# Optimization experiments

Hardware: AMD Instinct MI355X
Metric: run time of the kernel (lower is better)

The kernel has to match this reference:

```python
import jax, jax.numpy as jnp
import numpy as np

N = 25000; E = 100000; H = 64; NODE_IN = 32; EDGE_IN = 16; L = 3


def _lin(key, fan_in, fan_out):
    kw, kb = jax.random.split(key)
    s = 1.0 / np.sqrt(fan_in)
    W = jax.random.uniform(kw, (fan_out, fan_in), minval=-s, maxval=s, dtype=jnp.float32)
    b = jax.random.uniform(kb, (fan_out,), minval=-s, maxval=s, dtype=jnp.float32)
    return W, b


def setup_inputs() -> dict:
    key = jax.random.key(0)
    ks = jax.random.split(key, 16)
    x = jax.random.normal(ks[0], (N, NODE_IN), dtype=jnp.float32)
    edge_attr = jax.random.normal(ks[1], (E, EDGE_IN), dtype=jnp.float32)
    edge_index = jax.random.randint(ks[2], (2, E), 0, N, dtype=jnp.int32)
    Wn1, bn1 = _lin(ks[3], NODE_IN, H)
    Wn2, bn2 = _lin(ks[4], H, H)
    Wn3, bn3 = _lin(ks[5], H, H)
    We1, be1 = _lin(ks[6], EDGE_IN, H)
    We2, be2 = _lin(ks[7], H, H)
    We3, be3 = _lin(ks[8], H, H * H)
    roots = jax.random.normal(ks[9], (L, H, H), dtype=jnp.float32) / np.sqrt(H)
    conv_bias = jnp.zeros((L, H), dtype=jnp.float32)
    s = 1.0 / np.sqrt(H)
    gru_Wih = jax.random.uniform(ks[10], (3 * H, H), minval=-s, maxval=s, dtype=jnp.float32)
    gru_Whh = jax.random.uniform(ks[11], (3 * H, H), minval=-s, maxval=s, dtype=jnp.float32)
    gru_bih = jax.random.uniform(ks[12], (3 * H,), minval=-s, maxval=s, dtype=jnp.float32)
    gru_bhh = jax.random.uniform(ks[13], (3 * H,), minval=-s, maxval=s, dtype=jnp.float32)
    return dict(x=x, edge_attr=edge_attr,
                Wn1=Wn1, bn1=bn1, Wn2=Wn2, bn2=bn2, Wn3=Wn3, bn3=bn3,
                We1=We1, be1=be1, We2=We2, be2=be2, We3=We3, be3=be3,
                roots=roots, conv_bias=conv_bias,
                gru_Wih=gru_Wih, gru_Whh=gru_Whh, gru_bih=gru_bih, gru_bhh=gru_bhh,
                edge_index=edge_index)


def _mpnn_forward(x, edge_attr, Wn1, bn1, Wn2, bn2, Wn3, bn3,
                  We1, be1, We2, be2, We3, be3,
                  roots, conv_bias, gru_Wih, gru_Whh, gru_bih, gru_bhh, edge_index):
    src, dst = edge_index[0], edge_index[1]
    # mlp_in: Linear-ReLU-Linear-ReLU-Linear
    h = jax.nn.relu(x @ Wn1.T + bn1)
    h = jax.nn.relu(h @ Wn2.T + bn2)
    h = h @ Wn3.T + bn3  # [N, H]
    # edge MLP is shared across all NNConv layers and edge_attr is constant -> compute once
    ew = jax.nn.relu(edge_attr @ We1.T + be1)
    ew = jax.nn.relu(ew @ We2.T + be2)
    ew = (ew @ We3.T + be3).reshape(E, H, H)  # per-edge weight [E, in, out]
    hidden = jnp.zeros((x.shape[0], H), dtype=h.dtype)  # GRU hidden (1 layer)
    for l in range(L):
        # NNConv: message_e = h[src_e] @ W_e, scatter-add to dst, plus root term and bias
        msg = jnp.einsum('ei,eio->eo', h[src], ew)
        aggr = jax.ops.segment_sum(msg, dst, num_segments=N)
        m = aggr + h @ roots[l] + conv_bias[l]  # [N, H]
        # GRU step (seq_len=1, batch=N)
        gi = m @ gru_Wih.T + gru_bih
        gh = hidden @ gru_Whh.T + gru_bhh
        i_r, i_z, i_n = jnp.split(gi, 3, axis=-1)
        h_r, h_z, h_n = jnp.split(gh, 3, axis=-1)
        r = jax.nn.sigmoid(i_r + h_r)
        z = jax.nn.sigmoid(i_z + h_z)
        n = jnp.tanh(i_n + r * h_n)
        hidden = (1.0 - z) * n + z * hidden
        h = hidden  # output of 1-layer GRU == new hidden
    return h


def reference(x, edge_attr, Wn1, bn1, Wn2, bn2, Wn3, bn3,
              We1, be1, We2, be2, We3, be3,
              roots, conv_bias, gru_Wih, gru_Whh, gru_bih, gru_bhh, edge_index):
    return _mpnn_forward(x, edge_attr, Wn1, bn1, Wn2, bn2, Wn3, bn3,
                         We1, be1, We2, be2, We3, be3,
                         roots, conv_bias, gru_Wih, gru_Whh, gru_bih, gru_bhh, edge_index)
```

## Files before the change

### kernel.cpp

```cpp
#include <hip/hip_runtime.h>
#include <math.h>

#define NN 25000
#define NE 100000

typedef _Float16 f16;
typedef _Float16 half8 __attribute__((ext_vector_type(8)));
typedef float f32x4 __attribute__((ext_vector_type(4)));

__global__ __launch_bounds__(256) void prep_all(
    const float* __restrict__ Wn1, const float* __restrict__ Wn2,
    const float* __restrict__ Wn3, const float* __restrict__ We1,
    const float* __restrict__ We2, const float* __restrict__ Wih,
    const float* __restrict__ Whh, const float* __restrict__ We3,
    const float* __restrict__ be3, const float* __restrict__ roots,
    float* __restrict__ T, f16* __restrict__ Wf16, f16* __restrict__ root16,
    f16* __restrict__ Wih16, f16* __restrict__ Whh16)
{
    int f = blockIdx.x * 256 + threadIdx.x;
    if (f >= 318464) return;
    if (f < 15360) {
        if (f < 2048)       { int j = f;         T[f] = Wn1[(j & 63) * 32 + (j >> 6)]; }
        else if (f < 6144)  { int j = f - 2048;  T[f] = Wn2[(j & 63) * 64 + (j >> 6)]; }
        else if (f < 10240) { int j = f - 6144;  T[f] = Wn3[(j & 63) * 64 + (j >> 6)]; }
        else if (f < 11264) { int j = f - 10240; T[f] = We1[(j & 63) * 16 + (j >> 6)]; }
        else                { int j = f - 11264; T[f] = We2[(j & 63) * 64 + (j >> 6)]; }
    } else {
        int g = f - 15360;
        if (g < 266240) {
            if (g < 262144) Wf16[g] = (f16)We3[g];
            else {
                int j = g - 262144; int o = (j >> 6), k = j & 63;
                Wf16[g] = (f16)be3[k * 64 + o];
            }
        } else {
            int g2 = g - 266240;
            if (g2 < 12288) {
                int l = g2 >> 12, j = g2 & 4095, o = j >> 6, i = j & 63;
                root16[g2] = (f16)roots[l * 4096 + i * 64 + o];
            } else if (g2 < 24576) Wih16[g2 - 12288] = (f16)Wih[g2 - 12288];
            else                   Whh16[g2 - 24576] = (f16)Whh[g2 - 24576];
        }
    }
}

__global__ __launch_bounds__(256) void node_mlp(
    const float* __restrict__ x, const float* __restrict__ T,
    const float* __restrict__ bn1, const float* __restrict__ bn2,
    const float* __restrict__ bn3,
    float* __restrict__ hbuf, f16* __restrict__ h16, float* __restrict__ aggr)
{
    __shared__ float sx[4][8][32];
    __shared__ float sh1[4][8][64];
    const float* Wn1T = T;
    const float* Wn2T = T + 2048;
    const float* Wn3T = T + 6144;
    int w = threadIdx.x >> 6, lane = threadIdx.x & 63;
    int n0 = blockIdx.x * 32 + w * 8;
    if (n0 >= NN) return;
    #pragma unroll
    for (int jj = 0; jj < 4; ++jj) {
        int f = jj * 64 + lane;
        sx[w][f >> 5][f & 31] = x[(size_t)(n0 + (f >> 5)) * 32 + (f & 31)];
    }
    float a[8];
    #pragma unroll
    for (int j = 0; j < 8; ++j) a[j] = bn1[lane];
    for (int i = 0; i < 32; i += 4) {
        float4 bb[8];
        #pragma unroll
        for (int j = 0; j < 8; ++j) bb[j] = *(const float4*)&sx[w][j][i];
        #pragma unroll
        for (int ii = 0; ii < 4; ++ii) {
            float wv = Wn1T[(i + ii) * 64 + lane];
            #pragma unroll
            for (int j = 0; j < 8; ++j) a[j] += ((const float*)&bb[j])[ii] * wv;
        }
    }
    #pragma unroll
    for (int j = 0; j < 8; ++j) { sh1[w][j][lane] = fmaxf(a[j], 0.f); a[j] = bn2[lane]; }
    for (int i = 0; i < 64; i += 4) {
        float4 bb[8];
        #pragma unroll
        for (int j = 0; j < 8; ++j) bb[j] = *(const float4*)&sh1[w][j][i];
        #pragma unroll
        for (int ii = 0; ii < 4; ++ii) {
            float wv = Wn2T[(i + ii) * 64 + lane];
            #pragma unroll
            for (int j = 0; j < 8; ++j) a[j] += ((const float*)&bb[j])[ii] * wv;
        }
    }
    #pragma unroll
    for (int j = 0; j < 8; ++j) { sh1[w][j][lane] = fmaxf(a[j], 0.f); a[j] = bn3[lane]; }
    for (int i = 0; i < 64; i += 4) {
        float4 bb[8];
        #pragma unroll
        for (int j = 0; j < 8; ++j) bb[j] = *(const float4*)&sh1[w][j][i];
        #pragma unroll
        for (int ii = 0; ii < 4; ++ii) {
            float wv = Wn3T[(i + ii) * 64 + lane];
            #pragma unroll
            for (int j = 0; j < 8; ++j) a[j] += ((const float*)&bb[j])[ii] * wv;
        }
    }
    #pragma unroll
    for (int j = 0; j < 8; ++j) {
        size_t idx = (size_t)(n0 + j) * 64 + lane;
        hbuf[idx] = a[j];
        h16[idx]  = (f16)a[j];
        aggr[idx] = 0.f;
    }
}

__global__ __launch_bounds__(256) void edge_mlp(
    const float* __restrict__ ea, const float* __restrict__ T,
    const float* __restrict__ be1, const float* __restrict__ be2,
    f16* __restrict__ ew16)
{
    __shared__ float sa[4][8][16];
    __shared__ float st[4][8][64];
    const float* We1T = T + 10240;
    const float* We2T = T + 11264;
    int w = threadIdx.x >> 6, lane = threadIdx.x & 63;
    int e0 = blockIdx.x * 32 + w * 8;
    if (e0 >= NE) return;
    #pragma unroll
    for (int jj = 0; jj < 2; ++jj) {
        int f = jj * 64 + lane;
        sa[w][f >> 4][f & 15] = ea[(size_t)(e0 + (f >> 4)) * 16 + (f & 15)];
    }
    float a[8];
    #pragma unroll
    for (int j = 0; j < 8; ++j) a[j] = be1[lane];
    for (int i = 0; i < 16; i += 4) {
        float4 bb[8];
        #pragma unroll
        for (int j = 0; j < 8; ++j) bb[j] = *(const float4*)&sa[w][j][i];
        #pragma unroll
        for (int ii = 0; ii < 4; ++ii) {
            float wv = We1T[(i + ii) * 64 + lane];
            #pragma unroll
            for (int j = 0; j < 8; ++j) a[j] += ((const float*)&bb[j])[ii] * wv;
        }
    }
    #pragma unroll
    for (int j = 0; j < 8; ++j) { st[w][j][lane] = fmaxf(a[j], 0.f); a[j] = be2[lane]; }
    for (int i = 0; i < 64; i += 4) {
        float4 bb[8];
        #pragma unroll
        for (int j = 0; j < 8; ++j) bb[j] = *(const float4*)&st[w][j][i];
        #pragma unroll
        for (int ii = 0; ii < 4; ++ii) {
            float wv = We2T[(i + ii) * 64 + lane];
            #pragma unroll
            for (int j = 0; j < 8; ++j) a[j] += ((const float*)&bb[j])[ii] * wv;
        }
    }
    #pragma unroll
    for (int j = 0; j < 8; ++j)
        ew16[(size_t)(e0 + j) * 64 + lane] = (f16)fmaxf(a[j], 0.f);
}

__device__ __forceinline__ half8 splat8(f16 v)
{ half8 r = { v, v, v, v, v, v, v, v }; return r; }

__global__ __launch_bounds__(256) void msg_mfma(
    const f16* __restrict__ h16, const f16* __restrict__ ew16,
    const f16* __restrict__ Wf16, const int* __restrict__ edge_index,
    float* __restrict__ aggr)
{
    __shared__ f16 sh_h[128][72];
    __shared__ f16 sh_ring[4][4096];
    __shared__ int sh_dst[128];
    int t = threadIdx.x, lane = t & 63, wv = t >> 6;
    int e0 = blockIdx.x * 128;
    char* ringc = (char*)&sh_ring[0][0];

    const uint4* gW = (const uint4*)Wf16;
    uint4 r0 = gW[t], r1 = gW[256 + t], r2 = gW[512 + t], r3 = gW[768 + t];

    {
        int row = t >> 1, part = t & 1;
        int e = e0 + row;
        bool valid = e < NE;
        int ec = valid ? e : NE - 1;
        int src = edge_index[ec];
        const uint4* hp = (const uint4*)(h16 + (size_t)src * 64 + part * 32);
        const uint4* ep = (const uint4*)(ew16 + (size_t)ec * 64 + part * 32);
        uint4 z = make_uint4(0u, 0u, 0u, 0u);
        uint4 h0 = hp[0], h1 = hp[1], h2 = hp[2], h3 = hp[3];
        uint4 g0 = valid ? ep[0] : z;
        uint4 g1 = valid ? ep[1] : z;
        uint4 g2 = valid ? ep[2] : z;
        uint4 g3 = valid ? ep[3] : z;
        *(uint4*)&sh_h[row][part * 32]      = h0;
        *(uint4*)&sh_h[row][part * 32 + 8]  = h1;
        *(uint4*)&sh_h[row][part * 32 + 16] = h2;
        *(uint4*)&sh_h[row][part * 32 + 24] = h3;
        int rb = row * 128, key = (row & 7) << 4;
        *(uint4*)(ringc + rb + ((part * 64 +  0) ^ key)) = g0;
        *(uint4*)(ringc + rb + ((part * 64 + 16) ^ key)) = g1;
        *(uint4*)(ringc + rb + ((part * 64 + 32) ^ key)) = g2;
        *(uint4*)(ringc + rb + ((part * 64 + 48) ^ key)) = g3;
        if (lane < 32) {
            int e2 = e0 + wv * 32 + lane;
            sh_dst[wv * 32 + lane] = (e2 < NE) ? edge_index[NE + e2] : -1;
        }
    }
    __syncthreads();

    int r16 = lane & 15, kq = lane >> 4;

    half8 ev0[8], ev1[8];
    {
        int key = (r16 & 7) << 4;
        #pragma unroll
        for (int m = 0; m < 8; ++m) {
            int row = m * 16 + r16;
            ev0[m] = *(const half8*)(ringc + row * 128 + ((kq * 16) ^ key));
            ev1[m] = *(const half8*)(ringc + row * 128 + ((64 + kq * 16) ^ key));
        }
    }

    __syncthreads();

    int d0 = t * 16, d1 = 4096 + t * 16;
    int dsw0 = d0 ^ (((d0 >> 7) & 7) << 4);
    int dsw1 = d1 ^ (((d1 >> 7) & 7) << 4);

    *(uint4*)(ringc + dsw0) = r0;
    *(uint4*)(ringc + dsw1) = r1;
    *(uint4*)(ringc + 8192 + dsw0) = r2;
    *(uint4*)(ringc + 8192 + dsw1) = r3;
    r0 = gW[2 * 512 + t]; r1 = gW[2 * 512 + 256 + t];
    r2 = gW[3 * 512 + t]; r3 = gW[3 * 512 + 256 + t];
    __syncthreads();

    f32x4 acc[8];
    #pragma unroll
    for (int m = 0; m < 8; ++m) acc[m] = (f32x4){0, 0, 0, 0};

    int swzA = (kq << 4) ^ ((r16 & 7) << 4);
    int swzB = ((kq << 4) | 64) ^ ((r16 & 7) << 4);
    int colBase = wv * 2048 + r16 * 128;

    for (int i8 = 0; i8 < 8; ++i8) {
        half8 hM[8];
        #pragma unroll
        for (int m = 0; m < 8; ++m)
            hM[m] = *(const half8*)&sh_h[m * 16 + r16][i8 * 8];
        #pragma unroll
        for (int w2 = 0; w2 < 4; ++w2) {
            const char* pairR = ringc + (w2 & 1) * 16384 + colBase;
            #pragma unroll
            for (int s = 0; s < 2; ++s) {
                const char* bb = pairR + s * 8192;
                half8 bs0 = *(const half8*)(bb + swzA);
                half8 bs1 = *(const half8*)(bb + swzB);
                #pragma unroll
                for (int m = 0; m < 8; ++m) {
                    f16 hs = hM[m][w2 * 2 + s];
                    half8 a0 = ev0[m] * splat8(hs);
                    half8 a1 = ev1[m] * splat8(hs);
                    acc[m] = __builtin_amdgcn_mfma_f32_16x16x32_f16(a0, bs0, acc[m], 0, 0, 0);
                    acc[m] = __builtin_amdgcn_mfma_f32_16x16x32_f16(a1, bs1, acc[m], 0, 0, 0);
                }
            }
            char* wb = ringc + ((w2 + 1) & 1) * 16384;
            *(uint4*)(wb + dsw0) = r0;
            *(uint4*)(wb + dsw1) = r1;
            *(uint4*)(wb + 8192 + dsw0) = r2;
            *(uint4*)(wb + 8192 + dsw1) = r3;
            int jw = i8 * 4 + w2;
            int sA = jw * 2 + 4; if (sA > 64) sA = 64;
            int sB = jw * 2 + 5; if (sB > 64) sB = 64;
            r0 = gW[(size_t)sA * 512 + t]; r1 = gW[(size_t)sA * 512 + 256 + t];
            r2 = gW[(size_t)sB * 512 + t]; r3 = gW[(size_t)sB * 512 + 256 + t];
            __syncthreads();
        }
    }

    {
        const char* bb = ringc + colBase;
        half8 bs0 = *(const half8*)(bb + swzA);
        half8 bs1 = *(const half8*)(bb + swzB);
        #pragma unroll
        for (int m = 0; m < 8; ++m) {
            int row = m * 16 + r16;
            half8 a0 = *(const half8*)&sh_h[row][kq * 8];
            half8 a1 = *(const half8*)&sh_h[row][32 + kq * 8];
            acc[m] = __builtin_amdgcn_mfma_f32_16x16x32_f16(a0, bs0, acc[m], 0, 0, 0);
            acc[m] = __builtin_amdgcn_mfma_f32_16x16x32_f16(a1, bs1, acc[m], 0, 0, 0);
        }
    }

    #pragma unroll
    for (int m = 0; m < 8; ++m) {
        #pragma unroll
        for (int reg = 0; reg < 4; ++reg) {
            int e_l = m * 16 + kq * 4 + reg;
            int d = sh_dst[e_l];
            if (d >= 0)
                atomicAdd(aggr + (size_t)d * 64 + wv * 16 + r16, acc[m][reg]);
        }
    }
}

__global__ __launch_bounds__(64) void gru_mfma(
    float* __restrict__ aggr, float* __restrict__ hbuf, f16* __restrict__ h16,
    const f16* __restrict__ root16, const float* __restrict__ cbias,
    const f16* __restrict__ Wih16, const f16* __restrict__ Whh16,
    const float* __restrict__ bih, const float* __restrict__ bhh,
    float* __restrict__ out2, int first)
{
    __shared__ f16 sh[16][72];
    __shared__ f16 sm[16][72];
    int lane = threadIdx.x & 63;
    int n0 = blockIdx.x * 16;

    {
        int row = lane >> 2, part = lane & 3;
        int n = n0 + row;
        uint4 z = make_uint4(0u, 0u, 0u, 0u);
        const uint4* hp = (const uint4*)(h16 + (size_t)n * 64 + part * 16);
        uint4 v0 = (n < NN) ? hp[0] : z;
        uint4 v1 = (n < NN) ? hp[1] : z;
        *(uint4*)&sh[row][part * 16]     = v0;
        *(uint4*)&sh[row][part * 16 + 8] = v1;
    }

    int r16 = lane & 15, kq = lane >> 4;
    half8 ah0 = *(const half8*)&sh[r16][kq * 8];
    half8 ah1 = *(const half8*)&sh[r16][32 + kq * 8];
    int nodeBase = kq * 4;

    f32x4 accm[4];
    #pragma unroll
    for (int tt = 0; tt < 4; ++tt) {
        int o = tt * 16 + r16;
        float cb = cbias[o];
        #pragma unroll
        for (int reg = 0; reg < 4; ++reg) {
            int n = n0 + nodeBase + reg;
            float v = 0.f;
            if (n < NN) {
                size_t ix = (size_t)n * 64 + o;
                v = aggr[ix] + cb;
                aggr[ix] = 0.f;
            }
            accm[tt][reg] = v;
        }
    }
    #pragma unroll
    for (int tt = 0; tt < 4; ++tt) {
        const f16* bp = root16 + (size_t)(tt * 16 + r16) * 64 + kq * 8;
        half8 b0 = *(const half8*)bp;
        half8 b1 = *(const half8*)(bp + 32);
        accm[tt] = __builtin_amdgcn_mfma_f32_16x16x32_f16(ah0, b0, accm[tt], 0, 0, 0);
        accm[tt] = __builtin_amdgcn_mfma_f32_16x16x32_f16(ah1, b1, accm[tt], 0, 0, 0);
    }
    #pragma unroll
    for (int tt = 0; tt < 4; ++tt)
        #pragma unroll
        for (int reg = 0; reg < 4; ++reg)
            sm[nodeBase + reg][tt * 16 + r16] = (f16)accm[tt][reg];
    half8 am0 = *(const half8*)&sm[r16][kq * 8];
    half8 am1 = *(const half8*)&sm[r16][32 + kq * 8];

    f32x4 acc_rz[8], acc_in[4], acc_hn[4];
    #pragma unroll
    for (int tt = 0; tt < 8; ++tt) acc_rz[tt] = (f32x4){0, 0, 0, 0};
    #pragma unroll
    for (int tt = 0; tt < 4; ++tt) { acc_in[tt] = (f32x4){0, 0, 0, 0}; acc_hn[tt] = (f32x4){0, 0, 0, 0}; }

    #pragma unroll
    for (int tt = 0; tt < 8; ++tt) {
        const f16* bp = Wih16 + (size_t)(tt * 16 + r16) * 64 + kq * 8;
        half8 b0 = *(const half8*)bp;
        half8 b1 = *(const half8*)(bp + 32);
        acc_rz[tt] = __builtin_amdgcn_mfma_f32_16x16x32_f16(am0, b0, acc_rz[tt], 0, 0, 0);
        acc_rz[tt] = __builtin_amdgcn_mfma_f32_16x16x32_f16(am1, b1, acc_rz[tt], 0, 0, 0);
    }
    #pragma unroll
    for (int tt = 0; tt < 4; ++tt) {
        const f16* bp = Wih16 + (size_t)(128 + tt * 16 + r16) * 64 + kq * 8;
        half8 b0 = *(const half8*)bp;
        half8 b1 = *(const half8*)(bp + 32);
        acc_in[tt] = __builtin_amdgcn_mfma_f32_16x16x32_f16(am0, b0, acc_in[tt], 0, 0, 0);
        acc_in[tt] = __builtin_amdgcn_mfma_f32_16x16x32_f16(am1, b1, acc_in[tt], 0, 0, 0);
    }
    if (!first) {
        #pragma unroll
        for (int tt = 0; tt < 8; ++tt) {
            const f16* bp = Whh16 + (size_t)(tt * 16 + r16) * 64 + kq * 8;
            half8 b0 = *(const half8*)bp;
            half8 b1 = *(const half8*)(bp + 32);
            acc_rz[tt] = __builtin_amdgcn_mfma_f32_16x16x32_f16(ah0, b0, acc_rz[tt], 0, 0, 0);
            acc_rz[tt] = __builtin_amdgcn_mfma_f32_16x16x32_f16(ah1, b1, acc_rz[tt], 0, 0, 0);
        }
        #pragma unroll
        for (int tt = 0; tt < 4; ++tt) {
            const f16* bp = Whh16 + (size_t)(128 + tt * 16 + r16) * 64 + kq * 8;
            half8 b0 = *(const half8*)bp;
            half8 b1 = *(const half8*)(bp + 32);
            acc_hn[tt] = __builtin_amdgcn_mfma_f32_16x16x32_f16(ah0, b0, acc_hn[tt], 0, 0, 0);
            acc_hn[tt] = __builtin_amdgcn_mfma_f32_16x16x32_f16(ah1, b1, acc_hn[tt], 0, 0, 0);
        }
    }

    #pragma unroll
    for (int tt = 0; tt < 4; ++tt) {
        int o = tt * 16 + r16;
        float b_r = bih[o] + bhh[o];
        float b_z = bih[64 + o] + bhh[64 + o];
        float bin = bih[128 + o];
        float bhn = bhh[128 + o];
        #pragma unroll
        for (int reg = 0; reg < 4; ++reg) {
            int n = n0 + nodeBase + reg;
            if (n >= NN) continue;
            size_t ix = (size_t)n * 64 + o;
            float rv = 1.f / (1.f + expf(-(acc_rz[tt][reg] + b_r)));
            float zv = 1.f / (1.f + expf(-(acc_rz[4 + tt][reg] + b_z)));
            float hn_ = first ? bhn : (acc_hn[tt][reg] + bhn);
            float nv = tanhf(acc_in[tt][reg] + bin + rv * hn_);
            float hold = first ? 0.f : hbuf[ix];
            float outv = (1.f - zv) * nv + zv * hold;
            hbuf[ix] = outv;
            h16[ix]  = (f16)outv;
            if (out2) out2[ix] = outv;
        }
    }
}

extern "C" void kernel_launch(void* const* d_in, const int* in_sizes, int n_in,
                              void* d_out, int out_size, void* d_ws, size_t ws_size,
                              hipStream_t stream)
{
    const float* x   = (const float*)d_in[0];
    const float* ea  = (const float*)d_in[1];
    const float* Wn1 = (const float*)d_in[2];  const float* bn1 = (const float*)d_in[3];
    const float* Wn2 = (const float*)d_in[4];  const float* bn2 = (const float*)d_in[5];
    const float* Wn3 = (const float*)d_in[6];  const float* bn3 = (const float*)d_in[7];
    const float* We1 = (const float*)d_in[8];  const float* be1 = (const float*)d_in[9];
    const float* We2 = (const float*)d_in[10]; const float* be2 = (const float*)d_in[11];
    const float* We3 = (const float*)d_in[12]; const float* be3 = (const float*)d_in[13];
    const float* roots = (const float*)d_in[14];
    const float* cb    = (const float*)d_in[15];
    const float* Wih = (const float*)d_in[16]; const float* Whh = (const float*)d_in[17];
    const float* bih = (const float*)d_in[18]; const float* bhh = (const float*)d_in[19];
    const int*   ei  = (const int*)d_in[20];

    float* ws   = (float*)d_ws;
    float* hbuf = ws;
    float* aggr = hbuf + (size_t)NN * 64;
    float* Tbuf = aggr + (size_t)NN * 64;
    f16*   h16  = (f16*)(ws + 2 * (size_t)NN * 64 + 16384);
    f16*   ew16 = h16  + (size_t)NN * 64;
    f16*   Wf16 = ew16 + (size_t)NE * 64;
    f16*   root16 = Wf16 + 266240;
    f16*   Wih16  = root16 + 12288;
    f16*   Whh16  = Wih16 + 12288;

    prep_all<<<(318464 + 255) / 256, 256, 0, stream>>>(Wn1, Wn2, Wn3, We1, We2,
        Wih, Whh, We3, be3, roots, Tbuf, Wf16, root16, Wih16, Whh16);
    node_mlp<<<(NN + 31) / 32, 256, 0, stream>>>(x, Tbuf, bn1, bn2, bn3,
                                                 hbuf, h16, aggr);
    edge_mlp<<<NE / 32, 256, 0, stream>>>(ea, Tbuf, be1, be2, ew16);

    for (int l = 0; l < 3; ++l) {
        msg_mfma<<<(NE + 127) / 128, 256, 0, stream>>>(h16, ew16, Wf16, ei, aggr);
        gru_mfma<<<(NN + 15) / 16, 64, 0, stream>>>(aggr, hbuf, h16,
            root16 + (size_t)l * 4096, cb + (size_t)l * 64,
            Wih16, Whh16, bih, bhh,
            (l == 2) ? (float*)d_out : nullptr, (l == 0) ? 1 : 0);
    }
}
```

Baseline: 437.1 us.

## Retile msg_mfma warps into 64-row by 64-col K-split tiles and fuse node/edge MLPs

The message kernel changes its warp work split. Each warp used to cover all 128 edge rows for a 16-column output slice. Now each warp covers 64 rows by all 64 columns over half of the K dimension, so each B-fragment load from LDS feeds four MFMAs instead of one and the per-warp operand products are halved. The two K-halves are reduced through LDS before the atomic scatter, which adds two barriers and some LDS traffic. Separately, the node and edge MLP kernels are merged into one launch with a block-index branch, removing one launch and letting the two workloads overlap.

```diff
diff --git a/kernel.cpp b/kernel.cpp
--- a/kernel.cpp
+++ b/kernel.cpp
@@ -44,121 +44,120 @@
     }
 }
 
-__global__ __launch_bounds__(256) void node_mlp(
-    const float* __restrict__ x, const float* __restrict__ T,
+#define NODE_BLOCKS ((NN + 31) / 32)
+#define EDGE_BLOCKS (NE / 32)
+
+__global__ __launch_bounds__(256) void fused_mlp(
+    const float* __restrict__ x, const float* __restrict__ ea,
+    const float* __restrict__ T,
     const float* __restrict__ bn1, const float* __restrict__ bn2,
     const float* __restrict__ bn3,
-    float* __restrict__ hbuf, f16* __restrict__ h16, float* __restrict__ aggr)
-{
-    __shared__ float sx[4][8][32];
-    __shared__ float sh1[4][8][64];
-    const float* Wn1T = T;
-    const float* Wn2T = T + 2048;
-    const float* Wn3T = T + 6144;
-    int w = threadIdx.x >> 6, lane = threadIdx.x & 63;
-    int n0 = blockIdx.x * 32 + w * 8;
-    if (n0 >= NN) return;
-    #pragma unroll
-    for (int jj = 0; jj < 4; ++jj) {
-        int f = jj * 64 + lane;
-        sx[w][f >> 5][f & 31] = x[(size_t)(n0 + (f >> 5)) * 32 + (f & 31)];
-    }
-    float a[8];
-    #pragma unroll
-    for (int j = 0; j < 8; ++j) a[j] = bn1[lane];
-    for (int i = 0; i < 32; i += 4) {
-        float4 bb[8];
-        #pragma unroll
-        for (int j = 0; j < 8; ++j) bb[j] = *(const float4*)&sx[w][j][i];
-        #pragma unroll
-        for (int ii = 0; ii < 4; ++ii) {
-            float wv = Wn1T[(i + ii) * 64 + lane];
-            #pragma unroll
-            for (int j = 0; j < 8; ++j) a[j] += ((const float*)&bb[j])[ii] * wv;
-        }
-    }
-    #pragma unroll
-    for (int j = 0; j < 8; ++j) { sh1[w][j][lane] = fmaxf(a[j], 0.f); a[j] = bn2[lane]; }
-    for (int i = 0; i < 64; i += 4) {
-        float4 bb[8];
-        #pragma unroll
-        for (int j = 0; j < 8; ++j) bb[j] = *(const float4*)&sh1[w][j][i];
-        #pragma unroll
-        for (int ii = 0; ii < 4; ++ii) {
-            float wv = Wn2T[(i + ii) * 64 + lane];
-            #pragma unroll
-            for (int j = 0; j < 8; ++j) a[j] += ((const float*)&bb[j])[ii] * wv;
-        }
-    }
-    #pragma unroll
-    for (int j = 0; j < 8; ++j) { sh1[w][j][lane] = fmaxf(a[j], 0.f); a[j] = bn3[lane]; }
-    for (int i = 0; i < 64; i += 4) {
-        float4 bb[8];
-        #pragma unroll
-        for (int j = 0; j < 8; ++j) bb[j] = *(const float4*)&sh1[w][j][i];
-        #pragma unroll
-        for (int ii = 0; ii < 4; ++ii) {
-            float wv = Wn3T[(i + ii) * 64 + lane];
-            #pragma unroll
-            for (int j = 0; j < 8; ++j) a[j] += ((const float*)&bb[j])[ii] * wv;
-        }
-    }
-    #pragma unroll
-    for (int j = 0; j < 8; ++j) {
-        size_t idx = (size_t)(n0 + j) * 64 + lane;
-        hbuf[idx] = a[j];
-        h16[idx]  = (f16)a[j];
-        aggr[idx] = 0.f;
-    }
-}
-
-__global__ __launch_bounds__(256) void edge_mlp(
-    const float* __restrict__ ea, const float* __restrict__ T,
     const float* __restrict__ be1, const float* __restrict__ be2,
+    float* __restrict__ hbuf, f16* __restrict__ h16, float* __restrict__ aggr,
     f16* __restrict__ ew16)
 {
-    __shared__ float sa[4][8][16];
-    __shared__ float st[4][8][64];
-    const float* We1T = T + 10240;
-    const float* We2T = T + 11264;
+    __shared__ float s_in[4][8][32];
+    __shared__ float s_t[4][8][64];
     int w = threadIdx.x >> 6, lane = threadIdx.x & 63;
-    int e0 = blockIdx.x * 32 + w * 8;
-    if (e0 >= NE) return;
-    #pragma unroll
-    for (int jj = 0; jj < 2; ++jj) {
-        int f = jj * 64 + lane;
-        sa[w][f >> 4][f & 15] = ea[(size_t)(e0 + (f >> 4)) * 16 + (f & 15)];
-    }
-    float a[8];
-    #pragma unroll
-    for (int j = 0; j < 8; ++j) a[j] = be1[lane];
-    for (int i = 0; i < 16; i += 4) {
-        float4 bb[8];
-        #pragma unroll
-        for (int j = 0; j < 8; ++j) bb[j] = *(const float4*)&sa[w][j][i];
-        #pragma unroll
-        for (int ii = 0; ii < 4; ++ii) {
-            float wv = We1T[(i + ii) * 64 + lane];
-            #pragma unroll
-            for (int j = 0; j < 8; ++j) a[j] += ((const float*)&bb[j])[ii] * wv;
-        }
-    }
-    #pragma unroll
-    for (int j = 0; j < 8; ++j) { st[w][j][lane] = fmaxf(a[j], 0.f); a[j] = be2[lane]; }
-    for (int i = 0; i < 64; i += 4) {
-        float4 bb[8];
-        #pragma unroll
-        for (int j = 0; j < 8; ++j) bb[j] = *(const float4*)&st[w][j][i];
-        #pragma unroll
-        for (int ii = 0; ii < 4; ++ii) {
-            float wv = We2T[(i + ii) * 64 + lane];
-            #pragma unroll
-            for (int j = 0; j < 8; ++j) a[j] += ((const float*)&bb[j])[ii] * wv;
-        }
-    }
-    #pragma unroll
-    for (int j = 0; j < 8; ++j)
-        ew16[(size_t)(e0 + j) * 64 + lane] = (f16)fmaxf(a[j], 0.f);
+    if (blockIdx.x < NODE_BLOCKS) {
+        const float* Wn1T = T;
+        const float* Wn2T = T + 2048;
+        const float* Wn3T = T + 6144;
+        int n0 = blockIdx.x * 32 + w * 8;
+        if (n0 >= NN) return;
+        #pragma unroll
+        for (int jj = 0; jj < 4; ++jj) {
+            int f = jj * 64 + lane;
+            s_in[w][f >> 5][f & 31] = x[(size_t)(n0 + (f >> 5)) * 32 + (f & 31)];
+        }
+        float a[8];
+        #pragma unroll
+        for (int j = 0; j < 8; ++j) a[j] = bn1[lane];
+        for (int i = 0; i < 32; i += 4) {
+            float4 bb[8];
+            #pragma unroll
+            for (int j = 0; j < 8; ++j) bb[j] = *(const float4*)&s_in[w][j][i];
+            #pragma unroll
+            for (int ii = 0; ii < 4; ++ii) {
+                float wv = Wn1T[(i + ii) * 64 + lane];
+                #pragma unroll
+                for (int j = 0; j < 8; ++j) a[j] += ((const float*)&bb[j])[ii] * wv;
+            }
+        }
+        #pragma unroll
+        for (int j = 0; j < 8; ++j) { s_t[w][j][lane] = fmaxf(a[j], 0.f); a[j] = bn2[lane]; }
+        for (int i = 0; i < 64; i += 4) {
+            float4 bb[8];
+            #pragma unroll
+            for (int j = 0; j < 8; ++j) bb[j] = *(const float4*)&s_t[w][j][i];
+            #pragma unroll
+            for (int ii = 0; ii < 4; ++ii) {
+                float wv = Wn2T[(i + ii) * 64 + lane];
+                #pragma unroll
+                for (int j = 0; j < 8; ++j) a[j] += ((const float*)&bb[j])[ii] * wv;
+            }
+        }
+        #pragma unroll
+        for (int j = 0; j < 8; ++j) { s_t[w][j][lane] = fmaxf(a[j], 0.f); a[j] = bn3[lane]; }
+        for (int i = 0; i < 64; i += 4) {
+            float4 bb[8];
+            #pragma unroll
+            for (int j = 0; j < 8; ++j) bb[j] = *(const float4*)&s_t[w][j][i];
+            #pragma unroll
+            for (int ii = 0; ii < 4; ++ii) {
+                float wv = Wn3T[(i + ii) * 64 + lane];
+                #pragma unroll
+                for (int j = 0; j < 8; ++j) a[j] += ((const float*)&bb[j])[ii] * wv;
+            }
+        }
+        #pragma unroll
+        for (int j = 0; j < 8; ++j) {
+            size_t idx = (size_t)(n0 + j) * 64 + lane;
+            hbuf[idx] = a[j];
+            h16[idx]  = (f16)a[j];
+            aggr[idx] = 0.f;
+        }
+    } else {
+        const float* We1T = T + 10240;
+        const float* We2T = T + 11264;
+        int e0 = (blockIdx.x - NODE_BLOCKS) * 32 + w * 8;
+        if (e0 >= NE) return;
+        #pragma unroll
+        for (int jj = 0; jj < 2; ++jj) {
+            int f = jj * 64 + lane;
+            s_in[w][(f >> 4) & 7][f & 15] = ea[(size_t)(e0 + (f >> 4)) * 16 + (f & 15)];
+        }
+        float a[8];
+        #pragma unroll
+        for (int j = 0; j < 8; ++j) a[j] = be1[lane];
+        for (int i = 0; i < 16; i += 4) {
+            float4 bb[8];
+            #pragma unroll
+            for (int j = 0; j < 8; ++j) bb[j] = *(const float4*)&s_in[w][j][i];
+            #pragma unroll
+            for (int ii = 0; ii < 4; ++ii) {
+                float wv = We1T[(i + ii) * 64 + lane];
+                #pragma unroll
+                for (int j = 0; j < 8; ++j) a[j] += ((const float*)&bb[j])[ii] * wv;
+            }
+        }
+        #pragma unroll
+        for (int j = 0; j < 8; ++j) { s_t[w][j][lane] = fmaxf(a[j], 0.f); a[j] = be2[lane]; }
+        for (int i = 0; i < 64; i += 4) {
+            float4 bb[8];
+            #pragma unroll
+            for (int j = 0; j < 8; ++j) bb[j] = *(const float4*)&s_t[w][j][i];
+            #pragma unroll
+            for (int ii = 0; ii < 4; ++ii) {
+                float wv = We2T[(i + ii) * 64 + lane];
+                #pragma unroll
+                for (int j = 0; j < 8; ++j) a[j] += ((const float*)&bb[j])[ii] * wv;
+            }
+        }
+        #pragma unroll
+        for (int j = 0; j < 8; ++j)
+            ew16[(size_t)(e0 + j) * 64 + lane] = (f16)fmaxf(a[j], 0.f);
+    }
 }
 
 __device__ __forceinline__ half8 splat8(f16 v)
@@ -210,18 +209,17 @@
     __syncthreads();
 
     int r16 = lane & 15, kq = lane >> 4;
-
-    half8 ev0[8], ev1[8];
-    {
-        int key = (r16 & 7) << 4;
-        #pragma unroll
-        for (int m = 0; m < 8; ++m) {
-            int row = m * 16 + r16;
-            ev0[m] = *(const half8*)(ringc + row * 128 + ((kq * 16) ^ key));
-            ev1[m] = *(const half8*)(ringc + row * 128 + ((64 + kq * 16) ^ key));
-        }
-    }
-
+    int mg   = wv >> 1;
+    int koff = wv & 1;
+    int rowB = mg * 64;
+
+    half8 ev[4];
+    #pragma unroll
+    for (int m = 0; m < 4; ++m) {
+        int row = rowB + m * 16 + r16;
+        int key = (row & 7) << 4;
+        ev[m] = *(const half8*)(ringc + row * 128 + ((koff * 64 + kq * 16) ^ key));
+    }
     __syncthreads();
 
     int d0 = t * 16, d1 = 4096 + t * 16;
@@ -236,35 +234,51 @@
     r2 = gW[3 * 512 + t]; r3 = gW[3 * 512 + 256 + t];
     __syncthreads();
 
-    f32x4 acc[8];
-    #pragma unroll
-    for (int m = 0; m < 8; ++m) acc[m] = (f32x4){0, 0, 0, 0};
-
-    int swzA = (kq << 4) ^ ((r16 & 7) << 4);
-    int swzB = ((kq << 4) | 64) ^ ((r16 & 7) << 4);
-    int colBase = wv * 2048 + r16 * 128;
+    f32x4 acc[4][4];
+    #pragma unroll
+    for (int m = 0; m < 4; ++m)
+        #pragma unroll
+        for (int n = 0; n < 4; ++n) acc[m][n] = (f32x4){0, 0, 0, 0};
+
+    int swz = (koff * 64 + (kq << 4)) ^ ((r16 & 7) << 4);
 
     for (int i8 = 0; i8 < 8; ++i8) {
-        half8 hM[8];
-        #pragma unroll
-        for (int m = 0; m < 8; ++m)
-            hM[m] = *(const half8*)&sh_h[m * 16 + r16][i8 * 8];
+        half8 hM[4];
+        #pragma unroll
+        for (int m = 0; m < 4; ++m)
+            hM[m] = *(const half8*)&sh_h[rowB + m * 16 + r16][i8 * 8];
         #pragma unroll
         for (int w2 = 0; w2 < 4; ++w2) {
-            const char* pairR = ringc + (w2 & 1) * 16384 + colBase;
+            const char* pairR = ringc + (w2 & 1) * 16384;
             #pragma unroll
             for (int s = 0; s < 2; ++s) {
-                const char* bb = pairR + s * 8192;
-                half8 bs0 = *(const half8*)(bb + swzA);
-                half8 bs1 = *(const half8*)(bb + swzB);
-                #pragma unroll
-                for (int m = 0; m < 8; ++m) {
-                    f16 hs = hM[m][w2 * 2 + s];
-                    half8 a0 = ev0[m] * splat8(hs);
-                    half8 a1 = ev1[m] * splat8(hs);
-                    acc[m] = __builtin_amdgcn_mfma_f32_16x16x32_f16(a0, bs0, acc[m], 0, 0, 0);
-                    acc[m] = __builtin_amdgcn_mfma_f32_16x16x32_f16(a1, bs1, acc[m], 0, 0, 0);
-                }
+                const char* bb = pairR + s * 8192 + r16 * 128 + swz;
+                half8 bs0 = *(const half8*)(bb);
+                half8 bs1 = *(const half8*)(bb + 2048);
+                half8 bs2 = *(const half8*)(bb + 4096);
+                half8 bs3 = *(const half8*)(bb + 6144);
+                f16 hv0 = hM[0][w2 * 2 + s], hv1 = hM[1][w2 * 2 + s];
+                f16 hv2 = hM[2][w2 * 2 + s], hv3 = hM[3][w2 * 2 + s];
+                half8 a0 = ev[0] * splat8(hv0);
+                half8 a1 = ev[1] * splat8(hv1);
+                half8 a2 = ev[2] * splat8(hv2);
+                half8 a3 = ev[3] * splat8(hv3);
+                acc[0][0] = __builtin_amdgcn_mfma_f32_16x16x32_f16(a0, bs0, acc[0][0], 0, 0, 0);
+                acc[0][1] = __builtin_amdgcn_mfma_f32_16x16x32_f16(a0, bs1, acc[0][1], 0, 0, 0);
+                acc[0][2] = __builtin_amdgcn_mfma_f32_16x16x32_f16(a0, bs2, acc[0][2], 0, 0, 0);
+                acc[0][3] = __builtin_amdgcn_mfma_f32_16x16x32_f16(a0, bs3, acc[0][3], 0, 0, 0);
+                acc[1][0] = __builtin_amdgcn_mfma_f32_16x16x32_f16(a1, bs0, acc[1][0], 0, 0, 0);
+                acc[1][1] = __builtin_amdgcn_mfma_f32_16x16x32_f16(a1, bs1, acc[1][1], 0, 0, 0);
+                acc[1][2] = __builtin_amdgcn_mfma_f32_16x16x32_f16(a1, bs2, acc[1][2], 0, 0, 0);
+                acc[1][3] = __builtin_amdgcn_mfma_f32_16x16x32_f16(a1, bs3, acc[1][3], 0, 0, 0);
+                acc[2][0] = __builtin_amdgcn_mfma_f32_16x16x32_f16(a2, bs0, acc[2][0], 0, 0, 0);
+                acc[2][1] = __builtin_amdgcn_mfma_f32_16x16x32_f16(a2, bs1, acc[2][1], 0, 0, 0);
+                acc[2][2] = __builtin_amdgcn_mfma_f32_16x16x32_f16(a2, bs2, acc[2][2], 0, 0, 0);
+                acc[2][3] = __builtin_amdgcn_mfma_f32_16x16x32_f16(a2, bs3, acc[2][3], 0, 0, 0);
+                acc[3][0] = __builtin_amdgcn_mfma_f32_16x16x32_f16(a3, bs0, acc[3][0], 0, 0, 0);
+                acc[3][1] = __builtin_amdgcn_mfma_f32_16x16x32_f16(a3, bs1, acc[3][1], 0, 0, 0);
+                acc[3][2] = __builtin_amdgcn_mfma_f32_16x16x32_f16(a3, bs2, acc[3][2], 0, 0, 0);
+                acc[3][3] = __builtin_amdgcn_mfma_f32_16x16x32_f16(a3, bs3, acc[3][3], 0, 0, 0);
             }
             char* wb = ringc + ((w2 + 1) & 1) * 16384;
             *(uint4*)(wb + dsw0) = r0;
@@ -281,27 +295,48 @@
     }
 
     {
-        const char* bb = ringc + colBase;
-        half8 bs0 = *(const half8*)(bb + swzA);
-        half8 bs1 = *(const half8*)(bb + swzB);
-        #pragma unroll
-        for (int m = 0; m < 8; ++m) {
-            int row = m * 16 + r16;
-            half8 a0 = *(const half8*)&sh_h[row][kq * 8];
-            half8 a1 = *(const half8*)&sh_h[row][32 + kq * 8];
-            acc[m] = __builtin_amdgcn_mfma_f32_16x16x32_f16(a0, bs0, acc[m], 0, 0, 0);
-            acc[m] = __builtin_amdgcn_mfma_f32_16x16x32_f16(a1, bs1, acc[m], 0, 0, 0);
-        }
-    }
-
-    #pragma unroll
-    for (int m = 0; m < 8; ++m) {
-        #pragma unroll
-        for (int reg = 0; reg < 4; ++reg) {
-            int e_l = m * 16 + kq * 4 + reg;
-            int d = sh_dst[e_l];
-            if (d >= 0)
-                atomicAdd(aggr + (size_t)d * 64 + wv * 16 + r16, acc[m][reg]);
+        const char* bb = ringc + r16 * 128 + swz;
+        half8 bs0 = *(const half8*)(bb);
+        half8 bs1 = *(const half8*)(bb + 2048);
+        half8 bs2 = *(const half8*)(bb + 4096);
+        half8 bs3 = *(const half8*)(bb + 6144);
+        #pragma unroll
+        for (int m = 0; m < 4; ++m) {
+            half8 a = *(const half8*)&sh_h[rowB + m * 16 + r16][koff * 32 + kq * 8];
+            acc[m][0] = __builtin_amdgcn_mfma_f32_16x16x32_f16(a, bs0, acc[m][0], 0, 0, 0);
+            acc[m][1] = __builtin_amdgcn_mfma_f32_16x16x32_f16(a, bs1, acc[m][1], 0, 0, 0);
+            acc[m][2] = __builtin_amdgcn_mfma_f32_16x16x32_f16(a, bs2, acc[m][2], 0, 0, 0);
+            acc[m][3] = __builtin_amdgcn_mfma_f32_16x16x32_f16(a, bs3, acc[m][3], 0, 0, 0);
+        }
+    }
+    __syncthreads();
+
+    if (koff == 1) {
+        #pragma unroll
+        for (int m = 0; m < 4; ++m)
+            #pragma unroll
+            for (int n = 0; n < 4; ++n)
+                *(f32x4*)(ringc + mg * 16384 + (m * 4 + n) * 1024 + lane * 16) = acc[m][n];
+    }
+    __syncthreads();
+    if (koff == 0) {
+        #pragma unroll
+        for (int m = 0; m < 4; ++m) {
+            #pragma unroll
+            for (int n = 0; n < 4; ++n)
+                acc[m][n] += *(const f32x4*)(ringc + mg * 16384 + (m * 4 + n) * 1024 + lane * 16);
+            #pragma unroll
+            for (int reg = 0; reg < 4; ++reg) {
+                int e_l = mg * 64 + m * 16 + kq * 4 + reg;
+                int d = sh_dst[e_l];
+                if (d >= 0) {
+                    float* ap = aggr + (size_t)d * 64 + r16;
+                    atomicAdd(ap,      acc[m][0][reg]);
+                    atomicAdd(ap + 16, acc[m][1][reg]);
+                    atomicAdd(ap + 32, acc[m][2][reg]);
+                    atomicAdd(ap + 48, acc[m][3][reg]);
+                }
+            }
         }
     }
 }
@@ -464,9 +499,8 @@
 
     prep_all<<<(318464 + 255) / 256, 256, 0, stream>>>(Wn1, Wn2, Wn3, We1, We2,
         Wih, Whh, We3, be3, roots, Tbuf, Wf16, root16, Wih16, Whh16);
-    node_mlp<<<(NN + 31) / 32, 256, 0, stream>>>(x, Tbuf, bn1, bn2, bn3,
-                                                 hbuf, h16, aggr);
-    edge_mlp<<<NE / 32, 256, 0, stream>>>(ea, Tbuf, be1, be2, ew16);
+    fused_mlp<<<NODE_BLOCKS + EDGE_BLOCKS, 256, 0, stream>>>(x, ea, Tbuf,
+        bn1, bn2, bn3, be1, be2, hbuf, h16, aggr, ew16);
 
     for (int l = 0; l < 3; ++l) {
         msg_mfma<<<(NE + 127) / 128, 256, 0, stream>>>(h16, ew16, Wf16, ei, aggr);
```

New measurement: 400.9 us. -8.3%, faster.
